# Kernel tuning notes

Measured on AMD Instinct MI355X. Metric: run time of the kernel, lower is better.

The kernel has to match this reference:

```python
import jax, jax.numpy as jnp
import numpy as np

H = 256

def setup_inputs() -> dict:
    key = jax.random.key(0)
    ks = jax.random.split(key, 8)
    B, S = 32, 4096
    hidden = jax.random.normal(ks[0], (B, H), dtype=jnp.float32)
    encoder_outputs = jax.random.normal(ks[1], (B, S, H), dtype=jnp.float32)
    scale = 1.0 / np.sqrt(H)
    W1_w = jax.random.uniform(ks[2], (H, H), jnp.float32, -scale, scale)
    W1_b = jax.random.uniform(ks[3], (H,), jnp.float32, -scale, scale)
    W2_w = jax.random.uniform(ks[4], (H, H), jnp.float32, -scale, scale)
    W2_b = jax.random.uniform(ks[5], (H,), jnp.float32, -scale, scale)
    V_w = jax.random.uniform(ks[6], (H, 1), jnp.float32, -scale, scale)
    V_b = jax.random.uniform(ks[7], (1,), jnp.float32, -scale, scale)
    return {"hidden": hidden, "encoder_outputs": encoder_outputs,
            "W1_w": W1_w, "W1_b": W1_b, "W2_w": W2_w, "W2_b": W2_b,
            "V_w": V_w, "V_b": V_b}

def reference(hidden, encoder_outputs, W1_w, W1_b, W2_w, W2_b, V_w, V_b):
    # hidden: (B,H), encoder_outputs: (B,S,H)
    q = hidden @ W1_w + W1_b                     # (B,H)
    k = jnp.einsum('bsh,hd->bsd', encoder_outputs, W2_w) + W2_b  # (B,S,H)
    energy = jnp.tanh(q[:, None, :] + k)         # (B,S,H)
    scores = jnp.einsum('bsh,ho->bso', energy, V_w) + V_b        # (B,S,1)
    attention_weights = jax.nn.softmax(scores, axis=1)           # (B,S,1)
    context_vector = jnp.einsum('bso,bsh->bh', attention_weights, encoder_outputs)  # (B,H)
    return attention_weights, context_vector
```

## Files before the change

### kernel.cpp

```cpp
#include <hip/hip_runtime.h>
#include <hip/hip_bf16.h>
#include <math.h>

#define BB 32
#define SS 4096
#define HH 256

typedef __bf16 bf16x8 __attribute__((ext_vector_type(8)));
typedef float f32x4 __attribute__((ext_vector_type(4)));

#define GLOBAL_AS __attribute__((address_space(1)))
#define LDS_AS    __attribute__((address_space(3)))

__device__ inline bf16x8 cvt8(const float4& x, const float4& y) {
    union { __hip_bfloat162 p[4]; bf16x8 v; } u;
    u.p[0] = __float22bfloat162_rn(make_float2(x.x, x.y));
    u.p[1] = __float22bfloat162_rn(make_float2(x.z, x.w));
    u.p[2] = __float22bfloat162_rn(make_float2(y.x, y.y));
    u.p[3] = __float22bfloat162_rn(make_float2(y.z, y.w));
    return u.v;
}

__device__ inline float fast_tanh(float x) {
    float xc = fminf(fmaxf(x, -10.f), 10.f);
    float e  = __expf(2.f * xc);
    return (e - 1.f) * __builtin_amdgcn_rcpf(e + 1.f);
}

__global__ void prep_kernel(const float* __restrict__ W2_w,
                            ushort* __restrict__ w2sw,
                            const float* __restrict__ hidden,
                            const float* __restrict__ W1_w,
                            const float* __restrict__ W1_b,
                            const float* __restrict__ W2_b,
                            const float* __restrict__ V_w,
                            float* __restrict__ qq,
                            float* __restrict__ Mout) {
    __shared__ float red[HH];
    const int t = threadIdx.x;
    if (blockIdx.x < 256) {
        const int i = blockIdx.x * 256 + t;
        const int j    = i & 7;
        const int lane = (i >> 3) & 63;
        const int nt   = (i >> 9) & 15;
        const int kc   = i >> 13;
        const int k = kc * 32 + ((lane >> 4) & 3) * 8 + j;
        const int n = nt * 16 + (lane & 15);
        __hip_bfloat16 h = __float2bfloat16(W2_w[k * HH + n]);
        w2sw[i] = *(ushort*)&h;
    } else if (blockIdx.x < 256 + BB) {
        const int b = blockIdx.x - 256;
        red[t] = hidden[b * HH + t];
        __syncthreads();
        float acc = 0.f;
#pragma unroll 16
        for (int k = 0; k < HH; ++k)
            acc = fmaf(red[k], W1_w[k * HH + t], acc);
        qq[b * HH + t] = acc + W1_b[t] + W2_b[t];
    } else {
        red[t] = fabsf(V_w[t]);
        __syncthreads();
        for (int off = 128; off > 0; off >>= 1) {
            if (t < off) red[t] += red[t + off];
            __syncthreads();
        }
        if (t == 0) Mout[0] = red[0];
    }
}

__global__ __launch_bounds__(256, 4)
void score_ctx_kernel(const float* __restrict__ enc,
                      const ushort* __restrict__ w2sw,
                      const float* __restrict__ qq,
                      const float* __restrict__ V_w,
                      const float* __restrict__ Mptr,
                      float* __restrict__ wtilde,
                      float* __restrict__ part) {
    __shared__ ushort w2buf[2][8192];
    __shared__ float sc_lds[64];
    __shared__ float accl[4][HH];

    const int t    = threadIdx.x;
    const int b    = blockIdx.y;
    const int c    = blockIdx.x;
    const int s0   = c * 64;
    const int wave = t >> 6;
    const int lane = t & 63;
    const int mw   = wave & 1;
    const int nw   = wave >> 1;
    const int l15  = lane & 15;
    const int quad = lane >> 4;

    f32x4 acc[2][8];
#pragma unroll
    for (int mt = 0; mt < 2; ++mt)
#pragma unroll
        for (int nt = 0; nt < 8; ++nt) acc[mt][nt] = (f32x4)0.f;

    {
        const char* gsrc = (const char*)w2sw + t * 16;
        char* ldst = (char*)&w2buf[0][0] + wave * 1024;
#pragma unroll
        for (int i = 0; i < 4; ++i)
            __builtin_amdgcn_global_load_lds(
                (const GLOBAL_AS void*)(gsrc + i * 4096),
                (LDS_AS void*)(ldst + i * 4096), 16, 0, 0);
    }

    const float* aptr0 =
        enc + ((size_t)(b * SS + s0 + mw * 32 + l15)) * HH + quad * 8;
    const float* aptr1 = aptr0 + (size_t)16 * HH;
    float4 ax0 = *(const float4*)aptr0, ay0 = *(const float4*)(aptr0 + 4);
    float4 ax1 = *(const float4*)aptr1, ay1 = *(const float4*)(aptr1 + 4);

    for (int kc = 0; kc < 8; ++kc) {
        const int cur = kc & 1;
        __syncthreads();
        if (kc < 7) {
            const char* gsrc = (const char*)w2sw + (kc + 1) * 16384 + t * 16;
            char* ldst = (char*)&w2buf[cur ^ 1][0] + wave * 1024;
#pragma unroll
            for (int i = 0; i < 4; ++i)
                __builtin_amdgcn_global_load_lds(
                    (const GLOBAL_AS void*)(gsrc + i * 4096),
                    (LDS_AS void*)(ldst + i * 4096), 16, 0, 0);
        }
        bf16x8 af0 = cvt8(ax0, ay0);
        bf16x8 af1 = cvt8(ax1, ay1);
        if (kc < 7) {
            const int o = (kc + 1) * 32;
            ax0 = *(const float4*)(aptr0 + o);
            ay0 = *(const float4*)(aptr0 + o + 4);
            ax1 = *(const float4*)(aptr1 + o);
            ay1 = *(const float4*)(aptr1 + o + 4);
        }
#pragma unroll
        for (int nt = 0; nt < 8; ++nt) {
            bf16x8 bf =
                *(const bf16x8*)&w2buf[cur][((nw * 8 + nt) * 64 + lane) * 8];
            acc[0][nt] = __builtin_amdgcn_mfma_f32_16x16x32_bf16(af0, bf, acc[0][nt], 0, 0, 0);
            acc[1][nt] = __builtin_amdgcn_mfma_f32_16x16x32_bf16(af1, bf, acc[1][nt], 0, 0, 0);
        }
    }

    float p[2][4] = {{0.f, 0.f, 0.f, 0.f}, {0.f, 0.f, 0.f, 0.f}};
#pragma unroll
    for (int nt = 0; nt < 8; ++nt) {
        const int n = nw * 128 + nt * 16 + l15;
        const float qn = qq[b * HH + n];
        const float vn = V_w[n];
#pragma unroll
        for (int mt = 0; mt < 2; ++mt)
#pragma unroll
            for (int r = 0; r < 4; ++r)
                p[mt][r] = fmaf(vn, fast_tanh(qn + acc[mt][nt][r]), p[mt][r]);
    }
#pragma unroll
    for (int off = 1; off < 16; off <<= 1)
#pragma unroll
        for (int mt = 0; mt < 2; ++mt)
#pragma unroll
            for (int r = 0; r < 4; ++r)
                p[mt][r] += __shfl_xor(p[mt][r], off);

    if (nw == 0 && l15 == 0) {
#pragma unroll
        for (int mt = 0; mt < 2; ++mt)
            *(float4*)&sc_lds[mw * 32 + mt * 16 + quad * 4] =
                make_float4(p[mt][0], p[mt][1], p[mt][2], p[mt][3]);
    }
    __syncthreads();
    const float Mv = Mptr[0];
    if (nw == 1 && l15 == 0) {
#pragma unroll
        for (int mt = 0; mt < 2; ++mt) {
            const int row = mw * 32 + mt * 16 + quad * 4;
            float4 h = *(const float4*)&sc_lds[row];
            float4 v = make_float4(__expf(h.x + p[mt][0] - Mv),
                                   __expf(h.y + p[mt][1] - Mv),
                                   __expf(h.z + p[mt][2] - Mv),
                                   __expf(h.w + p[mt][3] - Mv));
            *(float4*)&sc_lds[row] = v;
            *(float4*)&wtilde[b * SS + s0 + row] = v;
        }
    }
    __syncthreads();

    const int tr = t >> 6;
    const int h0 = (t & 63) * 4;
    float4 a = make_float4(0.f, 0.f, 0.f, 0.f);
    const float* ep = enc + ((size_t)(b * SS + s0)) * HH;
#pragma unroll
    for (int jj = 0; jj < 16; ++jj) {
        const int j = jj * 4 + tr;
        const float4 e = *(const float4*)(ep + (size_t)j * HH + h0);
        const float w = sc_lds[j];
        a.x = fmaf(w, e.x, a.x);
        a.y = fmaf(w, e.y, a.y);
        a.z = fmaf(w, e.z, a.z);
        a.w = fmaf(w, e.w, a.w);
    }
    *(float4*)&accl[tr][h0] = a;
    __syncthreads();

    part[((size_t)(b * 64 + c)) * HH + t] =
        accl[0][t] + accl[1][t] + accl[2][t] + accl[3][t];
}

__global__ __launch_bounds__(256)
void finish_kernel(const float* __restrict__ wtilde,
                   const float* __restrict__ part,
                   float* __restrict__ weights_out,
                   float* __restrict__ ctx_out) {
    __shared__ float red[256];
    __shared__ float linv_s;
    const int b = blockIdx.x;
    const int t = threadIdx.x;

    const float4* wt4 = (const float4*)(wtilde + (size_t)b * SS);
    float4 vals[4];
    float l = 0.f;
#pragma unroll
    for (int i = 0; i < 4; ++i) {
        vals[i] = wt4[i * 256 + t];
        l += vals[i].x + vals[i].y + vals[i].z + vals[i].w;
    }
    red[t] = l;
    __syncthreads();
    for (int off = 128; off > 0; off >>= 1) {
        if (t < off) red[t] += red[t + off];
        __syncthreads();
    }
    if (t == 0) linv_s = 1.f / red[0];
    __syncthreads();
    const float linv = linv_s;

    float4* wo4 = (float4*)(weights_out + (size_t)b * SS);
#pragma unroll
    for (int i = 0; i < 4; ++i) {
        const float4 v = vals[i];
        wo4[i * 256 + t] =
            make_float4(v.x * linv, v.y * linv, v.z * linv, v.w * linv);
    }

    float a = 0.f;
#pragma unroll 8
    for (int c = 0; c < 64; ++c)
        a += part[((size_t)(b * 64 + c)) * HH + t];
    ctx_out[b * HH + t] = a * linv;
}

extern "C" void kernel_launch(void* const* d_in, const int* in_sizes, int n_in,
                              void* d_out, int out_size, void* d_ws, size_t ws_size,
                              hipStream_t stream) {
    const float* hidden = (const float*)d_in[0];
    const float* enc    = (const float*)d_in[1];
    const float* W1_w   = (const float*)d_in[2];
    const float* W1_b   = (const float*)d_in[3];
    const float* W2_w   = (const float*)d_in[4];
    const float* W2_b   = (const float*)d_in[5];
    const float* V_w    = (const float*)d_in[6];
    const float* V_b    = (const float*)d_in[7];
    (void)V_b;

    float* out_weights = (float*)d_out;
    float* out_ctx     = (float*)d_out + BB * SS;

    float* ws      = (float*)d_ws;
    float* ws_qq   = ws;
    float* ws_wt   = ws_qq + BB * HH;
    float* ws_part = ws_wt + BB * SS;
    float* ws_M    = ws_part + BB * 64 * HH;
    ushort* ws_w2  = (ushort*)(ws_M + 4);

    prep_kernel<<<dim3(256 + BB + 1), dim3(256), 0, stream>>>(
        W2_w, ws_w2, hidden, W1_w, W1_b, W2_b, V_w, ws_qq, ws_M);
    score_ctx_kernel<<<dim3(SS / 64, BB), dim3(256), 0, stream>>>(
        enc, ws_w2, ws_qq, V_w, ws_M, ws_wt, ws_part);
    finish_kernel<<<dim3(BB), dim3(256), 0, stream>>>(
        ws_wt, ws_part, out_weights, out_ctx);
}
```

Baseline: 244.6 us.

## Load full W2 into LDS once per 1024-thread block covering 512 rows

The score kernel now uses 1024-thread blocks that each stage the whole bf16 W2 (128KB) into LDS once and process 512 sequence rows. Each wave handles 16 rows with all 256 output columns, and the per-K-chunk double buffering and barriers are removed. The context partials shrink from 64 to 8 per batch, and tanh uses an exp2-based form without clamping. The cost is one block per CU with only 256 blocks in total, which lowers occupancy and latency hiding, and A-fragment loads are reused less across waves.

```diff
diff --git a/kernel.cpp b/kernel.cpp
--- a/kernel.cpp
+++ b/kernel.cpp
@@ -22,9 +22,8 @@
 }
 
 __device__ inline float fast_tanh(float x) {
-    float xc = fminf(fmaxf(x, -10.f), 10.f);
-    float e  = __expf(2.f * xc);
-    return (e - 1.f) * __builtin_amdgcn_rcpf(e + 1.f);
+    float e = __builtin_amdgcn_exp2f(x * 2.8853900817779268f);
+    return 1.f - 2.f * __builtin_amdgcn_rcpf(e + 1.f);
 }
 
 __global__ void prep_kernel(const float* __restrict__ W2_w,
@@ -68,7 +67,7 @@
     }
 }
 
-__global__ __launch_bounds__(256, 4)
+__global__ __launch_bounds__(1024)
 void score_ctx_kernel(const float* __restrict__ enc,
                       const ushort* __restrict__ w2sw,
                       const float* __restrict__ qq,
@@ -76,135 +75,107 @@
                       const float* __restrict__ Mptr,
                       float* __restrict__ wtilde,
                       float* __restrict__ part) {
-    __shared__ ushort w2buf[2][8192];
-    __shared__ float sc_lds[64];
-    __shared__ float accl[4][HH];
+    extern __shared__ char smem[];
+    ushort* w2buf = (ushort*)smem;
+    float*  ctxl  = (float*)(smem + 131072);
 
     const int t    = threadIdx.x;
     const int b    = blockIdx.y;
-    const int c    = blockIdx.x;
-    const int s0   = c * 64;
-    const int wave = t >> 6;
+    const int cx   = blockIdx.x;
+    const int wid  = t >> 6;
     const int lane = t & 63;
-    const int mw   = wave & 1;
-    const int nw   = wave >> 1;
     const int l15  = lane & 15;
     const int quad = lane >> 4;
 
-    f32x4 acc[2][8];
-#pragma unroll
-    for (int mt = 0; mt < 2; ++mt)
-#pragma unroll
-        for (int nt = 0; nt < 8; ++nt) acc[mt][nt] = (f32x4)0.f;
-
     {
         const char* gsrc = (const char*)w2sw + t * 16;
-        char* ldst = (char*)&w2buf[0][0] + wave * 1024;
-#pragma unroll
-        for (int i = 0; i < 4; ++i)
+        char* ldst = smem + wid * 1024;
+#pragma unroll
+        for (int i = 0; i < 8; ++i)
             __builtin_amdgcn_global_load_lds(
-                (const GLOBAL_AS void*)(gsrc + i * 4096),
-                (LDS_AS void*)(ldst + i * 4096), 16, 0, 0);
-    }
-
-    const float* aptr0 =
-        enc + ((size_t)(b * SS + s0 + mw * 32 + l15)) * HH + quad * 8;
-    const float* aptr1 = aptr0 + (size_t)16 * HH;
-    float4 ax0 = *(const float4*)aptr0, ay0 = *(const float4*)(aptr0 + 4);
-    float4 ax1 = *(const float4*)aptr1, ay1 = *(const float4*)(aptr1 + 4);
-
-    for (int kc = 0; kc < 8; ++kc) {
-        const int cur = kc & 1;
-        __syncthreads();
-        if (kc < 7) {
-            const char* gsrc = (const char*)w2sw + (kc + 1) * 16384 + t * 16;
-            char* ldst = (char*)&w2buf[cur ^ 1][0] + wave * 1024;
-#pragma unroll
-            for (int i = 0; i < 4; ++i)
-                __builtin_amdgcn_global_load_lds(
-                    (const GLOBAL_AS void*)(gsrc + i * 4096),
-                    (LDS_AS void*)(ldst + i * 4096), 16, 0, 0);
+                (const GLOBAL_AS void*)(gsrc + i * 16384),
+                (LDS_AS void*)(ldst + i * 16384), 16, 0, 0);
+    }
+
+    float qv[16], vv[16];
+#pragma unroll
+    for (int nt = 0; nt < 16; ++nt) {
+        qv[nt] = qq[b * HH + nt * 16 + l15];
+        vv[nt] = V_w[nt * 16 + l15];
+    }
+    const float Mv = Mptr[0];
+    float4 cacc = make_float4(0.f, 0.f, 0.f, 0.f);
+
+    __syncthreads();
+
+    for (int p = 0; p < 2; ++p) {
+        const int s0 = cx * 512 + p * 256 + wid * 16;
+        const float* rowp =
+            enc + ((size_t)(b * SS + s0 + l15)) * HH + (quad << 3);
+
+        f32x4 acc[16];
+#pragma unroll
+        for (int nt = 0; nt < 16; ++nt) acc[nt] = (f32x4)0.f;
+
+        float4 a0x = *(const float4*)rowp;
+        float4 a0y = *(const float4*)(rowp + 4);
+#pragma unroll
+        for (int kc = 0; kc < 8; ++kc) {
+            float4 a1x, a1y;
+            if (kc < 7) {
+                a1x = *(const float4*)(rowp + (kc + 1) * 32);
+                a1y = *(const float4*)(rowp + (kc + 1) * 32 + 4);
+            }
+            const bf16x8 af = cvt8(a0x, a0y);
+#pragma unroll
+            for (int nt = 0; nt < 16; ++nt) {
+                const bf16x8 bfr =
+                    *(const bf16x8*)&w2buf[((kc * 16 + nt) * 64 + lane) * 8];
+                acc[nt] = __builtin_amdgcn_mfma_f32_16x16x32_bf16(
+                    af, bfr, acc[nt], 0, 0, 0);
+            }
+            if (kc < 7) { a0x = a1x; a0y = a1y; }
         }
-        bf16x8 af0 = cvt8(ax0, ay0);
-        bf16x8 af1 = cvt8(ax1, ay1);
-        if (kc < 7) {
-            const int o = (kc + 1) * 32;
-            ax0 = *(const float4*)(aptr0 + o);
-            ay0 = *(const float4*)(aptr0 + o + 4);
-            ax1 = *(const float4*)(aptr1 + o);
-            ay1 = *(const float4*)(aptr1 + o + 4);
+
+        float p0[4] = {0.f, 0.f, 0.f, 0.f};
+#pragma unroll
+        for (int nt = 0; nt < 16; ++nt)
+#pragma unroll
+            for (int r = 0; r < 4; ++r)
+                p0[r] = fmaf(vv[nt], fast_tanh(qv[nt] + acc[nt][r]), p0[r]);
+#pragma unroll
+        for (int off = 1; off < 16; off <<= 1)
+#pragma unroll
+            for (int r = 0; r < 4; ++r)
+                p0[r] += __shfl_xor(p0[r], off);
+
+        float wv[4];
+#pragma unroll
+        for (int r = 0; r < 4; ++r) wv[r] = __expf(p0[r] - Mv);
+        if (l15 == 0)
+            *(float4*)&wtilde[(size_t)b * SS + s0 + quad * 4] =
+                make_float4(wv[0], wv[1], wv[2], wv[3]);
+
+        const float* ep = enc + ((size_t)(b * SS + s0)) * HH + (lane << 2);
+#pragma unroll
+        for (int j = 0; j < 16; ++j) {
+            const float wj = __shfl(wv[j & 3], (j >> 2) << 4);
+            const float4 e = *(const float4*)(ep + (size_t)j * HH);
+            cacc.x = fmaf(wj, e.x, cacc.x);
+            cacc.y = fmaf(wj, e.y, cacc.y);
+            cacc.z = fmaf(wj, e.z, cacc.z);
+            cacc.w = fmaf(wj, e.w, cacc.w);
         }
-#pragma unroll
-        for (int nt = 0; nt < 8; ++nt) {
-            bf16x8 bf =
-                *(const bf16x8*)&w2buf[cur][((nw * 8 + nt) * 64 + lane) * 8];
-            acc[0][nt] = __builtin_amdgcn_mfma_f32_16x16x32_bf16(af0, bf, acc[0][nt], 0, 0, 0);
-            acc[1][nt] = __builtin_amdgcn_mfma_f32_16x16x32_bf16(af1, bf, acc[1][nt], 0, 0, 0);
-        }
-    }
-
-    float p[2][4] = {{0.f, 0.f, 0.f, 0.f}, {0.f, 0.f, 0.f, 0.f}};
-#pragma unroll
-    for (int nt = 0; nt < 8; ++nt) {
-        const int n = nw * 128 + nt * 16 + l15;
-        const float qn = qq[b * HH + n];
-        const float vn = V_w[n];
-#pragma unroll
-        for (int mt = 0; mt < 2; ++mt)
-#pragma unroll
-            for (int r = 0; r < 4; ++r)
-                p[mt][r] = fmaf(vn, fast_tanh(qn + acc[mt][nt][r]), p[mt][r]);
-    }
-#pragma unroll
-    for (int off = 1; off < 16; off <<= 1)
-#pragma unroll
-        for (int mt = 0; mt < 2; ++mt)
-#pragma unroll
-            for (int r = 0; r < 4; ++r)
-                p[mt][r] += __shfl_xor(p[mt][r], off);
-
-    if (nw == 0 && l15 == 0) {
-#pragma unroll
-        for (int mt = 0; mt < 2; ++mt)
-            *(float4*)&sc_lds[mw * 32 + mt * 16 + quad * 4] =
-                make_float4(p[mt][0], p[mt][1], p[mt][2], p[mt][3]);
-    }
-    __syncthreads();
-    const float Mv = Mptr[0];
-    if (nw == 1 && l15 == 0) {
-#pragma unroll
-        for (int mt = 0; mt < 2; ++mt) {
-            const int row = mw * 32 + mt * 16 + quad * 4;
-            float4 h = *(const float4*)&sc_lds[row];
-            float4 v = make_float4(__expf(h.x + p[mt][0] - Mv),
-                                   __expf(h.y + p[mt][1] - Mv),
-                                   __expf(h.z + p[mt][2] - Mv),
-                                   __expf(h.w + p[mt][3] - Mv));
-            *(float4*)&sc_lds[row] = v;
-            *(float4*)&wtilde[b * SS + s0 + row] = v;
-        }
-    }
-    __syncthreads();
-
-    const int tr = t >> 6;
-    const int h0 = (t & 63) * 4;
-    float4 a = make_float4(0.f, 0.f, 0.f, 0.f);
-    const float* ep = enc + ((size_t)(b * SS + s0)) * HH;
-#pragma unroll
-    for (int jj = 0; jj < 16; ++jj) {
-        const int j = jj * 4 + tr;
-        const float4 e = *(const float4*)(ep + (size_t)j * HH + h0);
-        const float w = sc_lds[j];
-        a.x = fmaf(w, e.x, a.x);
-        a.y = fmaf(w, e.y, a.y);
-        a.z = fmaf(w, e.z, a.z);
-        a.w = fmaf(w, e.w, a.w);
-    }
-    *(float4*)&accl[tr][h0] = a;
-    __syncthreads();
-
-    part[((size_t)(b * 64 + c)) * HH + t] =
-        accl[0][t] + accl[1][t] + accl[2][t] + accl[3][t];
+    }
+
+    *(float4*)&ctxl[wid * HH + (lane << 2)] = cacc;
+    __syncthreads();
+    if (t < HH) {
+        float s = 0.f;
+#pragma unroll
+        for (int w = 0; w < 16; ++w) s += ctxl[w * HH + t];
+        part[((size_t)(b * 8 + cx)) * HH + t] = s;
+    }
 }
 
 __global__ __launch_bounds__(256)
@@ -244,9 +215,9 @@
     }
 
     float a = 0.f;
-#pragma unroll 8
-    for (int c = 0; c < 64; ++c)
-        a += part[((size_t)(b * 64 + c)) * HH + t];
+#pragma unroll
+    for (int c = 0; c < 8; ++c)
+        a += part[((size_t)(b * 8 + c)) * HH + t];
     ctx_out[b * HH + t] = a * linv;
 }
 
@@ -273,9 +244,17 @@
     float* ws_M    = ws_part + BB * 64 * HH;
     ushort* ws_w2  = (ushort*)(ws_M + 4);
 
+    static bool attr_done = false;
+    if (!attr_done) {
+        hipFuncSetAttribute(reinterpret_cast<const void*>(score_ctx_kernel),
+                            hipFuncAttributeMaxDynamicSharedMemorySize,
+                            147456);
+        attr_done = true;
+    }
+
     prep_kernel<<<dim3(256 + BB + 1), dim3(256), 0, stream>>>(
         W2_w, ws_w2, hidden, W1_w, W1_b, W2_b, V_w, ws_qq, ws_M);
-    score_ctx_kernel<<<dim3(SS / 64, BB), dim3(256), 0, stream>>>(
+    score_ctx_kernel<<<dim3(SS / 512, BB), dim3(1024), 147456, stream>>>(
         enc, ws_w2, ws_qq, V_w, ws_M, ws_wt, ws_part);
     finish_kernel<<<dim3(BB), dim3(256), 0, stream>>>(
         ws_wt, ws_part, out_weights, out_ctx);
```

Result: slower. 612.8 us (+150.5%).

## Stage encoder tiles into LDS via async loads and simplify tanh

Applied to the files above, without the earlier changes.

Encoder-output A-tiles now travel through a double-buffered LDS stage using global_load_lds next to the W2 tiles, instead of register prefetch. The loop waits with explicit vmcnt and barriers, and is fully unrolled. This overlaps global loads with MFMA work and lowers register pressure. fast_tanh drops the clamp and uses exp2 with a 1-2/(e+1) form, which gives fewer instructions but relies on rcp behaving well at overflow.

```diff
diff --git a/kernel.cpp b/kernel.cpp
--- a/kernel.cpp
+++ b/kernel.cpp
@@ -22,9 +22,8 @@
 }
 
 __device__ inline float fast_tanh(float x) {
-    float xc = fminf(fmaxf(x, -10.f), 10.f);
-    float e  = __expf(2.f * xc);
-    return (e - 1.f) * __builtin_amdgcn_rcpf(e + 1.f);
+    float e = __builtin_amdgcn_exp2f(x * 2.8853900817779268f);
+    return 1.f - 2.f * __builtin_amdgcn_rcpf(e + 1.f);
 }
 
 __global__ void prep_kernel(const float* __restrict__ W2_w,
@@ -76,7 +75,8 @@
                       const float* __restrict__ Mptr,
                       float* __restrict__ wtilde,
                       float* __restrict__ part) {
-    __shared__ ushort w2buf[2][8192];
+    __shared__ __align__(16) ushort w2buf[2][8192];
+    __shared__ __align__(16) float  abuf[2][2048];
     __shared__ float sc_lds[64];
     __shared__ float accl[4][HH];
 
@@ -91,57 +91,67 @@
     const int l15  = lane & 15;
     const int quad = lane >> 4;
 
+    const float* encA = enc + ((size_t)(b * SS + s0)) * HH;
+    const int arow  = wave * 16 + (lane >> 3);
+    const int acolf = (lane & 7) * 4;
+
+#define STAGE(KC, NXT)                                                        \
+    do {                                                                      \
+        const char* gw_ = (const char*)w2sw + (KC) * 16384 + t * 16;          \
+        char* lw_ = (char*)&w2buf[(NXT)][0] + wave * 1024;                    \
+        _Pragma("unroll")                                                     \
+        for (int i_ = 0; i_ < 4; ++i_)                                        \
+            __builtin_amdgcn_global_load_lds(                                 \
+                (const GLOBAL_AS void*)(gw_ + i_ * 4096),                     \
+                (LDS_AS void*)(lw_ + i_ * 4096), 16, 0, 0);                   \
+        _Pragma("unroll")                                                     \
+        for (int i_ = 0; i_ < 2; ++i_)                                        \
+            __builtin_amdgcn_global_load_lds(                                 \
+                (const GLOBAL_AS void*)(encA + (size_t)(arow + i_ * 8) * HH + \
+                                        (KC) * 32 + acolf),                   \
+                (LDS_AS void*)((char*)&abuf[(NXT)][0] + wave * 2048 +         \
+                               i_ * 1024), 16, 0, 0);                         \
+    } while (0)
+
     f32x4 acc[2][8];
 #pragma unroll
     for (int mt = 0; mt < 2; ++mt)
 #pragma unroll
         for (int nt = 0; nt < 8; ++nt) acc[mt][nt] = (f32x4)0.f;
 
-    {
-        const char* gsrc = (const char*)w2sw + t * 16;
-        char* ldst = (char*)&w2buf[0][0] + wave * 1024;
-#pragma unroll
-        for (int i = 0; i < 4; ++i)
-            __builtin_amdgcn_global_load_lds(
-                (const GLOBAL_AS void*)(gsrc + i * 4096),
-                (LDS_AS void*)(ldst + i * 4096), 16, 0, 0);
-    }
-
-    const float* aptr0 =
-        enc + ((size_t)(b * SS + s0 + mw * 32 + l15)) * HH + quad * 8;
-    const float* aptr1 = aptr0 + (size_t)16 * HH;
-    float4 ax0 = *(const float4*)aptr0, ay0 = *(const float4*)(aptr0 + 4);
-    float4 ax1 = *(const float4*)aptr1, ay1 = *(const float4*)(aptr1 + 4);
-
+    STAGE(0, 0);
+
+#pragma unroll
     for (int kc = 0; kc < 8; ++kc) {
         const int cur = kc & 1;
-        __syncthreads();
         if (kc < 7) {
-            const char* gsrc = (const char*)w2sw + (kc + 1) * 16384 + t * 16;
-            char* ldst = (char*)&w2buf[cur ^ 1][0] + wave * 1024;
-#pragma unroll
-            for (int i = 0; i < 4; ++i)
-                __builtin_amdgcn_global_load_lds(
-                    (const GLOBAL_AS void*)(gsrc + i * 4096),
-                    (LDS_AS void*)(ldst + i * 4096), 16, 0, 0);
-        }
-        bf16x8 af0 = cvt8(ax0, ay0);
-        bf16x8 af1 = cvt8(ax1, ay1);
-        if (kc < 7) {
-            const int o = (kc + 1) * 32;
-            ax0 = *(const float4*)(aptr0 + o);
-            ay0 = *(const float4*)(aptr0 + o + 4);
-            ax1 = *(const float4*)(aptr1 + o);
-            ay1 = *(const float4*)(aptr1 + o + 4);
-        }
+            STAGE(kc + 1, cur ^ 1);
+            asm volatile("s_waitcnt vmcnt(6)" ::: "memory");
+        } else {
+            asm volatile("s_waitcnt vmcnt(0)" ::: "memory");
+        }
+        __builtin_amdgcn_s_barrier();
+
+        const int r0 = mw * 32 + l15;
+        const float4 ax0 = *(const float4*)&abuf[cur][r0 * 32 + quad * 8];
+        const float4 ay0 = *(const float4*)&abuf[cur][r0 * 32 + quad * 8 + 4];
+        const float4 ax1 = *(const float4*)&abuf[cur][(r0 + 16) * 32 + quad * 8];
+        const float4 ay1 = *(const float4*)&abuf[cur][(r0 + 16) * 32 + quad * 8 + 4];
+        const bf16x8 af0 = cvt8(ax0, ay0);
+        const bf16x8 af1 = cvt8(ax1, ay1);
 #pragma unroll
         for (int nt = 0; nt < 8; ++nt) {
-            bf16x8 bf =
+            const bf16x8 bfr =
                 *(const bf16x8*)&w2buf[cur][((nw * 8 + nt) * 64 + lane) * 8];
-            acc[0][nt] = __builtin_amdgcn_mfma_f32_16x16x32_bf16(af0, bf, acc[0][nt], 0, 0, 0);
-            acc[1][nt] = __builtin_amdgcn_mfma_f32_16x16x32_bf16(af1, bf, acc[1][nt], 0, 0, 0);
-        }
-    }
+            acc[0][nt] = __builtin_amdgcn_mfma_f32_16x16x32_bf16(
+                af0, bfr, acc[0][nt], 0, 0, 0);
+            acc[1][nt] = __builtin_amdgcn_mfma_f32_16x16x32_bf16(
+                af1, bfr, acc[1][nt], 0, 0, 0);
+        }
+        asm volatile("s_waitcnt lgkmcnt(0)" ::: "memory");
+        __builtin_amdgcn_s_barrier();
+    }
+#undef STAGE
 
     float p[2][4] = {{0.f, 0.f, 0.f, 0.f}, {0.f, 0.f, 0.f, 0.f}};
 #pragma unroll
```

New measurement: 262.5 us. 1.07x slower.
